# Kernel optimization log

Hardware: AMD Instinct MI355X
Metric: run time of the kernel (lower is better)

## Reference

```python
import jax, jax.numpy as jnp
import numpy as np

B, S, H, F, E, K = 4, 2048, 1024, 2048, 8, 2


def setup_inputs() -> dict:
    key = jax.random.key(0)
    ks = jax.random.split(key, 5)
    scale = 0.02
    return {
        "hidden_states": jax.random.normal(ks[0], (B, S, H), dtype=jnp.float32),
        "gate_w": jax.random.normal(ks[1], (E, H), dtype=jnp.float32) * scale,
        "w1": jax.random.normal(ks[2], (E, F, H), dtype=jnp.float32) * scale,
        "w3": jax.random.normal(ks[3], (E, F, H), dtype=jnp.float32) * scale,
        "w2": jax.random.normal(ks[4], (E, H, F), dtype=jnp.float32) * scale,
    }


def reference(hidden_states, gate_w, w1, w3, w2):
    b, s, h = hidden_states.shape
    x = hidden_states.reshape(-1, h)  # [T, H]
    T = x.shape[0]
    # router
    router_logits = x @ gate_w.T  # [T, E]
    probs = jax.nn.softmax(router_logits.astype(jnp.float32), axis=-1)
    routing_weights, selected = jax.lax.top_k(probs, K)  # [T, K]
    routing_weights = routing_weights / jnp.sum(routing_weights, axis=-1, keepdims=True)
    routing_weights = routing_weights.astype(x.dtype)
    # dense per-token expert weight matrix [T, E] (zero for unselected experts)
    full_w = jnp.zeros((T, gate_w.shape[0]), dtype=x.dtype)
    full_w = full_w.at[jnp.arange(T)[:, None], selected].set(routing_weights)
    out = jnp.zeros_like(x)
    for e in range(gate_w.shape[0]):
        gated = jax.nn.silu(x @ w1[e].T) * (x @ w3[e].T)  # [T, F]
        y = gated @ w2[e].T  # [T, H]
        out = out + full_w[:, e:e + 1] * y
    return out.reshape(b, s, h), router_logits
```

## Files before the change

kernel.cpp:

```cpp
#include <hip/hip_runtime.h>

typedef unsigned short ushort_t;
typedef __attribute__((ext_vector_type(8))) short short8;
typedef __attribute__((ext_vector_type(4))) float floatx4;

#define T_TOK 8192
#define HDIM 1024
#define FDIM 2048
#define NEXP 8
#define TK_SLOTS (T_TOK * 2)
#define SORT_THREADS 1024
#define PER_THREAD (TK_SLOTS / SORT_THREADS)

__device__ __forceinline__ float b2f(unsigned short u) {
    union { unsigned int i; float f; } x; x.i = ((unsigned int)u) << 16; return x.f;
}
__device__ __forceinline__ unsigned short f2b(float f) {
    unsigned int u = __float_as_uint(f);
    u += 0x7FFF + ((u >> 16) & 1);
    return (unsigned short)(u >> 16);
}
__device__ __forceinline__ void gload16(const void* g, void* l) {
    __builtin_amdgcn_global_load_lds((const __attribute__((address_space(1))) void*)g,
                                     (__attribute__((address_space(3))) void*)l,
                                     16, 0, 0);
}

__global__ __launch_bounds__(256) void cvt_kernel(
    const float* __restrict__ src, ushort_t* __restrict__ dst, int n8)
{
    int i = blockIdx.x * 256 + threadIdx.x;
    if (i >= n8) return;
    const float4* s4 = (const float4*)src;
    float4 a = s4[2 * i], b = s4[2 * i + 1];
    short8 o;
    o[0] = (short)f2b(a.x); o[1] = (short)f2b(a.y);
    o[2] = (short)f2b(a.z); o[3] = (short)f2b(a.w);
    o[4] = (short)f2b(b.x); o[5] = (short)f2b(b.y);
    o[6] = (short)f2b(b.z); o[7] = (short)f2b(b.w);
    *(short8*)&dst[(size_t)i * 8] = o;
}

__global__ __launch_bounds__(256) void router_kernel(
    const float* __restrict__ X, const float* __restrict__ GW,
    float* __restrict__ logits_out, int* __restrict__ tk_e,
    float* __restrict__ tk_w)
{
    __shared__ __align__(16) float gw[NEXP * HDIM];
    const int tid = threadIdx.x;
#pragma unroll
    for (int c = 0; c < 8; ++c) {
        int idx = (c * 256 + tid) * 4;
        *(float4*)&gw[idx] = *(const float4*)&GW[idx];
    }
    __syncthreads();
    const int w = tid >> 6, l = tid & 63;
    const int t = blockIdx.x * 4 + w;
    float acc[NEXP];
#pragma unroll
    for (int e = 0; e < NEXP; ++e) acc[e] = 0.f;
#pragma unroll
    for (int it = 0; it < 4; ++it) {
        const int colb = it * 256 + l * 4;
        float4 xv = *(const float4*)&X[(size_t)t * HDIM + colb];
#pragma unroll
        for (int e = 0; e < NEXP; ++e) {
            float4 gv = *(const float4*)&gw[e * HDIM + colb];
            acc[e] += xv.x * gv.x + xv.y * gv.y + xv.z * gv.z + xv.w * gv.w;
        }
    }
#pragma unroll
    for (int off = 32; off >= 1; off >>= 1)
#pragma unroll
        for (int e = 0; e < NEXP; ++e) acc[e] += __shfl_xor(acc[e], off, 64);

    if (l == 0) {
        float mx = acc[0];
#pragma unroll
        for (int e = 1; e < NEXP; ++e) mx = fmaxf(mx, acc[e]);
        float p[NEXP];
#pragma unroll
        for (int e = 0; e < NEXP; ++e) p[e] = __expf(acc[e] - mx);
        int e0 = 0;
#pragma unroll
        for (int e = 1; e < NEXP; ++e) if (p[e] > p[e0]) e0 = e;
        int e1 = (e0 == 0) ? 1 : 0;
#pragma unroll
        for (int e = 0; e < NEXP; ++e) if (e != e0 && p[e] > p[e1]) e1 = e;
        float den = p[e0] + p[e1];
        tk_e[t * 2] = e0; tk_e[t * 2 + 1] = e1;
        tk_w[t * 2] = p[e0] / den; tk_w[t * 2 + 1] = p[e1] / den;
#pragma unroll
        for (int e = 0; e < NEXP; ++e) logits_out[(size_t)t * NEXP + e] = acc[e];
    }
}

__global__ __launch_bounds__(SORT_THREADS) void sort_kernel(
    const int* __restrict__ tk_e, const float* __restrict__ tk_w,
    int* __restrict__ counts, int* __restrict__ offsets,
    int* __restrict__ token_list, float* __restrict__ weight_list,
    int* __restrict__ slot_of)
{
    __shared__ int hist[NEXP][SORT_THREADS];
    __shared__ int offs[NEXP];
    const int thr = threadIdx.x;
    const int base = thr * PER_THREAD;

    int ev[PER_THREAD];
    int cnt[NEXP];
#pragma unroll
    for (int e = 0; e < NEXP; ++e) cnt[e] = 0;
#pragma unroll
    for (int i = 0; i < PER_THREAD; ++i) {
        ev[i] = tk_e[base + i];
#pragma unroll
        for (int e = 0; e < NEXP; ++e) cnt[e] += (ev[i] == e);
    }
#pragma unroll
    for (int e = 0; e < NEXP; ++e) hist[e][thr] = cnt[e];
    __syncthreads();

    for (int off = 1; off < SORT_THREADS; off <<= 1) {
        int v[NEXP];
#pragma unroll
        for (int e = 0; e < NEXP; ++e) v[e] = (thr >= off) ? hist[e][thr - off] : 0;
        __syncthreads();
#pragma unroll
        for (int e = 0; e < NEXP; ++e) hist[e][thr] += v[e];
        __syncthreads();
    }

    if (thr == 0) {
        int s = 0;
#pragma unroll
        for (int e = 0; e < NEXP; ++e) {
            int c = hist[e][SORT_THREADS - 1];
            offs[e] = s; offsets[e] = s; counts[e] = c; s += c;
        }
    }
    __syncthreads();

    int run[NEXP];
#pragma unroll
    for (int e = 0; e < NEXP; ++e) run[e] = offs[e] + hist[e][thr] - cnt[e];

#pragma unroll
    for (int i = 0; i < PER_THREAD; ++i) {
        int e = ev[i];
        int slot = 0;
#pragma unroll
        for (int ee = 0; ee < NEXP; ++ee) if (e == ee) slot = run[ee]++;
        token_list[slot] = (base + i) >> 1;
        weight_list[slot] = tk_w[base + i];
        slot_of[base + i] = slot;
    }
}

template <int MODE, int NDIM, int KDIM, bool GATHER>
__global__ __launch_bounds__(256) void moe_gemm(
    const ushort_t* __restrict__ A, const ushort_t* __restrict__ W,
    const int* __restrict__ counts, const int* __restrict__ offsets,
    const int* __restrict__ token_list, const float* __restrict__ weight_list,
    const ushort_t* C1, ushort_t* Out)
{
    const int e = blockIdx.z;
    const int ne = counts[e];
    const int m0 = blockIdx.y * 128;
    if (m0 >= ne) return;
    const int n0 = blockIdx.x * 128;
    const int aoff = offsets[e];
    const ushort_t* Bw = W + (size_t)e * NDIM * KDIM;

    __shared__ __align__(16) ushort_t As[128 * 32];
    __shared__ __align__(16) ushort_t Bs[128 * 32];

    const int tid = threadIdx.x;
    const int l = tid & 63;
    const int wv = tid >> 6;
    const int wm = wv >> 1, wn = wv & 1;
    const int quad = l >> 4, tl = l & 15;

    floatx4 acc[4][4];
#pragma unroll
    for (int i = 0; i < 4; ++i)
#pragma unroll
        for (int j = 0; j < 4; ++j)
#pragma unroll
            for (int r = 0; r < 4; ++r) acc[i][j][r] = 0.f;

    const ushort_t* agp[2];
    const ushort_t* bgp[2];
    ushort_t* alds[2];
    ushort_t* blds[2];
#pragma unroll
    for (int c = 0; c < 2; ++c) {
        int chunk = c * 256 + tid;
        int row = chunk >> 2, cc = chunk & 3;
        int rowc = m0 + row; if (rowc >= ne) rowc = ne - 1;
        size_t arow = GATHER ? (size_t)token_list[aoff + rowc] : (size_t)(aoff + rowc);
        agp[c] = A + arow * KDIM + cc * 8;
        bgp[c] = Bw + (size_t)(n0 + row) * KDIM + cc * 8;
        int base = (c * 256 + (tid & ~63)) * 8;
        alds[c] = &As[base];
        blds[c] = &Bs[base];
    }

    for (int k0 = 0; k0 < KDIM; k0 += 32) {
        gload16(agp[0] + k0, alds[0]);
        gload16(agp[1] + k0, alds[1]);
        gload16(bgp[0] + k0, blds[0]);
        gload16(bgp[1] + k0, blds[1]);
        __syncthreads();
        short8 a[4], b[4];
#pragma unroll
        for (int i = 0; i < 4; ++i)
            a[i] = *(const short8*)&As[(wm * 64 + i * 16 + tl) * 32 + quad * 8];
#pragma unroll
        for (int j = 0; j < 4; ++j)
            b[j] = *(const short8*)&Bs[(wn * 64 + j * 16 + tl) * 32 + quad * 8];
#pragma unroll
        for (int i = 0; i < 4; ++i)
#pragma unroll
            for (int j = 0; j < 4; ++j)
                acc[i][j] = __builtin_amdgcn_mfma_f32_16x16x32_bf16(a[i], b[j], acc[i][j], 0, 0, 0);
        __syncthreads();
    }

#pragma unroll
    for (int i = 0; i < 4; ++i) {
        int mrow = m0 + wm * 64 + i * 16 + quad * 4;
#pragma unroll
        for (int r = 0; r < 4; ++r) {
            int m = mrow + r;
            if (m < ne) {
                float wgt = 0.f;
                if constexpr (MODE == 2) wgt = weight_list[aoff + m];
#pragma unroll
                for (int j = 0; j < 4; ++j) {
                    int col = n0 + wn * 64 + j * 16 + tl;
                    size_t oidx = (size_t)(aoff + m) * NDIM + col;
                    float v = acc[i][j][r];
                    if constexpr (MODE == 0) {
                        float s = v / (1.f + __expf(-v));
                        Out[oidx] = f2b(s);
                    } else if constexpr (MODE == 1) {
                        float c = b2f(C1[oidx]);
                        Out[oidx] = f2b(v * c);
                    } else {
                        Out[oidx] = f2b(wgt * v);
                    }
                }
            }
        }
    }
}

__global__ __launch_bounds__(256) void combine_kernel(
    const ushort_t* __restrict__ Y, const int* __restrict__ slot_of,
    float* __restrict__ OutF)
{
    int idx = blockIdx.x * 256 + threadIdx.x;
    int t = idx >> 7;
    int h8 = (idx & 127) << 3;
    int s0 = slot_of[t * 2], s1 = slot_of[t * 2 + 1];
    short8 y0 = *(const short8*)&Y[(size_t)s0 * HDIM + h8];
    short8 y1 = *(const short8*)&Y[(size_t)s1 * HDIM + h8];
    float4 o0, o1;
    o0.x = b2f((unsigned short)y0[0]) + b2f((unsigned short)y1[0]);
    o0.y = b2f((unsigned short)y0[1]) + b2f((unsigned short)y1[1]);
    o0.z = b2f((unsigned short)y0[2]) + b2f((unsigned short)y1[2]);
    o0.w = b2f((unsigned short)y0[3]) + b2f((unsigned short)y1[3]);
    o1.x = b2f((unsigned short)y0[4]) + b2f((unsigned short)y1[4]);
    o1.y = b2f((unsigned short)y0[5]) + b2f((unsigned short)y1[5]);
    o1.z = b2f((unsigned short)y0[6]) + b2f((unsigned short)y1[6]);
    o1.w = b2f((unsigned short)y0[7]) + b2f((unsigned short)y1[7]);
    float4* dst = (float4*)&OutF[(size_t)t * HDIM + h8];
    dst[0] = o0; dst[1] = o1;
}

extern "C" void kernel_launch(void* const* d_in, const int* in_sizes, int n_in,
                              void* d_out, int out_size, void* d_ws, size_t ws_size,
                              hipStream_t stream)
{
    const float* X  = (const float*)d_in[0];
    const float* GW = (const float*)d_in[1];
    const float* W1 = (const float*)d_in[2];
    const float* W3 = (const float*)d_in[3];
    const float* W2 = (const float*)d_in[4];
    float* OUT = (float*)d_out;
    float* LOGITS = OUT + (size_t)T_TOK * HDIM;

    char* p = (char*)d_ws;
    auto take = [&](size_t b) { char* q = p; p += (b + 255) & ~(size_t)255; return q; };
    ushort_t* Xb = (ushort_t*)take((size_t)T_TOK * HDIM * 2);
    ushort_t* Wb = (ushort_t*)take((size_t)NEXP * FDIM * HDIM * 2);
    ushort_t* C1 = (ushort_t*)take((size_t)TK_SLOTS * FDIM * 2);
    ushort_t* Yb = (ushort_t*)take((size_t)TK_SLOTS * HDIM * 2);
    int*   counts      = (int*)take(NEXP * 4);
    int*   offsets     = (int*)take(NEXP * 4);
    int*   tk_e        = (int*)take(TK_SLOTS * 4);
    float* tk_w        = (float*)take(TK_SLOTS * 4);
    int*   slot_of     = (int*)take(TK_SLOTS * 4);
    int*   token_list  = (int*)take(TK_SLOTS * 4);
    float* weight_list = (float*)take(TK_SLOTS * 4);

    router_kernel<<<T_TOK / 4, 256, 0, stream>>>(X, GW, LOGITS, tk_e, tk_w);
    sort_kernel<<<1, SORT_THREADS, 0, stream>>>(tk_e, tk_w, counts, offsets,
                                                token_list, weight_list, slot_of);
    cvt_kernel<<<(T_TOK * HDIM / 8) / 256, 256, 0, stream>>>(X, Xb, T_TOK * HDIM / 8);

    cvt_kernel<<<(NEXP * FDIM * HDIM / 8) / 256, 256, 0, stream>>>(W1, Wb, NEXP * FDIM * HDIM / 8);
    moe_gemm<0, FDIM, HDIM, true ><<<dim3(FDIM / 128, T_TOK / 128, NEXP), 256, 0, stream>>>(
        Xb, Wb, counts, offsets, token_list, nullptr, nullptr, C1);

    cvt_kernel<<<(NEXP * FDIM * HDIM / 8) / 256, 256, 0, stream>>>(W3, Wb, NEXP * FDIM * HDIM / 8);
    moe_gemm<1, FDIM, HDIM, true ><<<dim3(FDIM / 128, T_TOK / 128, NEXP), 256, 0, stream>>>(
        Xb, Wb, counts, offsets, token_list, nullptr, C1, C1 );

    cvt_kernel<<<(NEXP * HDIM * FDIM / 8) / 256, 256, 0, stream>>>(W2, Wb, NEXP * HDIM * FDIM / 8);
    moe_gemm<2, HDIM, FDIM, false><<<dim3(HDIM / 128, T_TOK / 128, NEXP), 256, 0, stream>>>(
        C1 , Wb, counts, offsets, token_list, weight_list, nullptr, Yb);

    combine_kernel<<<(T_TOK * HDIM / 8) / 256, 256, 0, stream>>>(Yb, slot_of, OUT);
}
```

Measured before the change: 621.6 us.

## Fuse gate/up GEMMs into one kernel and scatter down-proj via atomics

```diff
diff --git a/kernel.cpp b/kernel.cpp
--- a/kernel.cpp
+++ b/kernel.cpp
@@ -24,6 +24,9 @@
     __builtin_amdgcn_global_load_lds((const __attribute__((address_space(1))) void*)g,
                                      (__attribute__((address_space(3))) void*)l,
                                      16, 0, 0);
+}
+__device__ __forceinline__ void atomAddF(float* p, float v) {
+    __hip_atomic_fetch_add(p, v, __ATOMIC_RELAXED, __HIP_MEMORY_SCOPE_AGENT);
 }
 
 __global__ __launch_bounds__(256) void cvt_kernel(
@@ -98,8 +101,7 @@
 __global__ __launch_bounds__(SORT_THREADS) void sort_kernel(
     const int* __restrict__ tk_e, const float* __restrict__ tk_w,
     int* __restrict__ counts, int* __restrict__ offsets,
-    int* __restrict__ token_list, float* __restrict__ weight_list,
-    int* __restrict__ slot_of)
+    int* __restrict__ token_list, float* __restrict__ weight_list)
 {
     __shared__ int hist[NEXP][SORT_THREADS];
     __shared__ int offs[NEXP];
@@ -152,16 +154,14 @@
         for (int ee = 0; ee < NEXP; ++ee) if (e == ee) slot = run[ee]++;
         token_list[slot] = (base + i) >> 1;
         weight_list[slot] = tk_w[base + i];
-        slot_of[base + i] = slot;
-    }
-}
-
-template <int MODE, int NDIM, int KDIM, bool GATHER>
-__global__ __launch_bounds__(256) void moe_gemm(
-    const ushort_t* __restrict__ A, const ushort_t* __restrict__ W,
+    }
+}
+
+__global__ __launch_bounds__(256) void moe_gemm13(
+    const ushort_t* __restrict__ A, const ushort_t* __restrict__ W1b,
+    const ushort_t* __restrict__ W3b,
     const int* __restrict__ counts, const int* __restrict__ offsets,
-    const int* __restrict__ token_list, const float* __restrict__ weight_list,
-    const ushort_t* C1, ushort_t* Out)
+    const int* __restrict__ token_list, ushort_t* __restrict__ G)
 {
     const int e = blockIdx.z;
     const int ne = counts[e];
@@ -169,10 +169,12 @@
     if (m0 >= ne) return;
     const int n0 = blockIdx.x * 128;
     const int aoff = offsets[e];
-    const ushort_t* Bw = W + (size_t)e * NDIM * KDIM;
+    const ushort_t* B1w = W1b + (size_t)e * FDIM * HDIM;
+    const ushort_t* B3w = W3b + (size_t)e * FDIM * HDIM;
 
     __shared__ __align__(16) ushort_t As[128 * 32];
-    __shared__ __align__(16) ushort_t Bs[128 * 32];
+    __shared__ __align__(16) ushort_t B1s[128 * 32];
+    __shared__ __align__(16) ushort_t B3s[128 * 32];
 
     const int tid = threadIdx.x;
     const int l = tid & 63;
@@ -180,6 +182,106 @@
     const int wm = wv >> 1, wn = wv & 1;
     const int quad = l >> 4, tl = l & 15;
 
+    floatx4 acc1[4][4], acc3[4][4];
+#pragma unroll
+    for (int i = 0; i < 4; ++i)
+#pragma unroll
+        for (int j = 0; j < 4; ++j)
+#pragma unroll
+            for (int r = 0; r < 4; ++r) { acc1[i][j][r] = 0.f; acc3[i][j][r] = 0.f; }
+
+    const ushort_t* agp[2];
+    const ushort_t* b1gp[2];
+    const ushort_t* b3gp[2];
+    ushort_t* alds[2];
+    ushort_t* b1lds[2];
+    ushort_t* b3lds[2];
+#pragma unroll
+    for (int c = 0; c < 2; ++c) {
+        int chunk = c * 256 + tid;
+        int row = chunk >> 2, cc = chunk & 3;
+        int rowc = m0 + row; if (rowc >= ne) rowc = ne - 1;
+        size_t arow = (size_t)token_list[aoff + rowc];
+        agp[c]  = A   + arow * HDIM + cc * 8;
+        b1gp[c] = B1w + (size_t)(n0 + row) * HDIM + cc * 8;
+        b3gp[c] = B3w + (size_t)(n0 + row) * HDIM + cc * 8;
+        int base = (c * 256 + (tid & ~63)) * 8;
+        alds[c]  = &As[base];
+        b1lds[c] = &B1s[base];
+        b3lds[c] = &B3s[base];
+    }
+
+    for (int k0 = 0; k0 < HDIM; k0 += 32) {
+        gload16(agp[0]  + k0, alds[0]);
+        gload16(agp[1]  + k0, alds[1]);
+        gload16(b1gp[0] + k0, b1lds[0]);
+        gload16(b1gp[1] + k0, b1lds[1]);
+        gload16(b3gp[0] + k0, b3lds[0]);
+        gload16(b3gp[1] + k0, b3lds[1]);
+        __syncthreads();
+        short8 a[4], b1[4], b3[4];
+#pragma unroll
+        for (int i = 0; i < 4; ++i)
+            a[i] = *(const short8*)&As[(wm * 64 + i * 16 + tl) * 32 + quad * 8];
+#pragma unroll
+        for (int j = 0; j < 4; ++j) {
+            b1[j] = *(const short8*)&B1s[(wn * 64 + j * 16 + tl) * 32 + quad * 8];
+            b3[j] = *(const short8*)&B3s[(wn * 64 + j * 16 + tl) * 32 + quad * 8];
+        }
+#pragma unroll
+        for (int i = 0; i < 4; ++i)
+#pragma unroll
+            for (int j = 0; j < 4; ++j) {
+                acc1[i][j] = __builtin_amdgcn_mfma_f32_16x16x32_bf16(a[i], b1[j], acc1[i][j], 0, 0, 0);
+                acc3[i][j] = __builtin_amdgcn_mfma_f32_16x16x32_bf16(a[i], b3[j], acc3[i][j], 0, 0, 0);
+            }
+        __syncthreads();
+    }
+
+#pragma unroll
+    for (int i = 0; i < 4; ++i) {
+        int mrow = m0 + wm * 64 + i * 16 + quad * 4;
+#pragma unroll
+        for (int r = 0; r < 4; ++r) {
+            int m = mrow + r;
+            if (m < ne) {
+#pragma unroll
+                for (int j = 0; j < 4; ++j) {
+                    int col = n0 + wn * 64 + j * 16 + tl;
+                    size_t oidx = (size_t)(aoff + m) * FDIM + col;
+                    float v1 = acc1[i][j][r];
+                    float v3 = acc3[i][j][r];
+                    float s = v1 / (1.f + __expf(-v1));
+                    G[oidx] = f2b(s * v3);
+                }
+            }
+        }
+    }
+}
+
+__global__ __launch_bounds__(256) void moe_gemm2(
+    const ushort_t* __restrict__ A , const ushort_t* __restrict__ W2b,
+    const int* __restrict__ counts, const int* __restrict__ offsets,
+    const int* __restrict__ token_list, const float* __restrict__ weight_list,
+    float* __restrict__ OUT)
+{
+    const int e = blockIdx.z;
+    const int ne = counts[e];
+    const int m0 = blockIdx.y * 128;
+    if (m0 >= ne) return;
+    const int n0 = blockIdx.x * 128;
+    const int aoff = offsets[e];
+    const ushort_t* Bw = W2b + (size_t)e * HDIM * FDIM;
+
+    __shared__ __align__(16) ushort_t As[128 * 32];
+    __shared__ __align__(16) ushort_t Bs[128 * 32];
+
+    const int tid = threadIdx.x;
+    const int l = tid & 63;
+    const int wv = tid >> 6;
+    const int wm = wv >> 1, wn = wv & 1;
+    const int quad = l >> 4, tl = l & 15;
+
     floatx4 acc[4][4];
 #pragma unroll
     for (int i = 0; i < 4; ++i)
@@ -197,15 +299,14 @@
         int chunk = c * 256 + tid;
         int row = chunk >> 2, cc = chunk & 3;
         int rowc = m0 + row; if (rowc >= ne) rowc = ne - 1;
-        size_t arow = GATHER ? (size_t)token_list[aoff + rowc] : (size_t)(aoff + rowc);
-        agp[c] = A + arow * KDIM + cc * 8;
-        bgp[c] = Bw + (size_t)(n0 + row) * KDIM + cc * 8;
+        agp[c] = A  + (size_t)(aoff + rowc) * FDIM + cc * 8;
+        bgp[c] = Bw + (size_t)(n0 + row) * FDIM + cc * 8;
         int base = (c * 256 + (tid & ~63)) * 8;
         alds[c] = &As[base];
         blds[c] = &Bs[base];
     }
 
-    for (int k0 = 0; k0 < KDIM; k0 += 32) {
+    for (int k0 = 0; k0 < FDIM; k0 += 32) {
         gload16(agp[0] + k0, alds[0]);
         gload16(agp[1] + k0, alds[1]);
         gload16(bgp[0] + k0, blds[0]);
@@ -233,49 +334,17 @@
         for (int r = 0; r < 4; ++r) {
             int m = mrow + r;
             if (m < ne) {
-                float wgt = 0.f;
-                if constexpr (MODE == 2) wgt = weight_list[aoff + m];
+                float wgt = weight_list[aoff + m];
+                int tok = token_list[aoff + m];
+                float* orow = OUT + (size_t)tok * HDIM;
 #pragma unroll
                 for (int j = 0; j < 4; ++j) {
                     int col = n0 + wn * 64 + j * 16 + tl;
-                    size_t oidx = (size_t)(aoff + m) * NDIM + col;
-                    float v = acc[i][j][r];
-                    if constexpr (MODE == 0) {
-                        float s = v / (1.f + __expf(-v));
-                        Out[oidx] = f2b(s);
-                    } else if constexpr (MODE == 1) {
-                        float c = b2f(C1[oidx]);
-                        Out[oidx] = f2b(v * c);
-                    } else {
-                        Out[oidx] = f2b(wgt * v);
-                    }
+                    atomAddF(&orow[col], wgt * acc[i][j][r]);
                 }
             }
         }
     }
-}
-
-__global__ __launch_bounds__(256) void combine_kernel(
-    const ushort_t* __restrict__ Y, const int* __restrict__ slot_of,
-    float* __restrict__ OutF)
-{
-    int idx = blockIdx.x * 256 + threadIdx.x;
-    int t = idx >> 7;
-    int h8 = (idx & 127) << 3;
-    int s0 = slot_of[t * 2], s1 = slot_of[t * 2 + 1];
-    short8 y0 = *(const short8*)&Y[(size_t)s0 * HDIM + h8];
-    short8 y1 = *(const short8*)&Y[(size_t)s1 * HDIM + h8];
-    float4 o0, o1;
-    o0.x = b2f((unsigned short)y0[0]) + b2f((unsigned short)y1[0]);
-    o0.y = b2f((unsigned short)y0[1]) + b2f((unsigned short)y1[1]);
-    o0.z = b2f((unsigned short)y0[2]) + b2f((unsigned short)y1[2]);
-    o0.w = b2f((unsigned short)y0[3]) + b2f((unsigned short)y1[3]);
-    o1.x = b2f((unsigned short)y0[4]) + b2f((unsigned short)y1[4]);
-    o1.y = b2f((unsigned short)y0[5]) + b2f((unsigned short)y1[5]);
-    o1.z = b2f((unsigned short)y0[6]) + b2f((unsigned short)y1[6]);
-    o1.w = b2f((unsigned short)y0[7]) + b2f((unsigned short)y1[7]);
-    float4* dst = (float4*)&OutF[(size_t)t * HDIM + h8];
-    dst[0] = o0; dst[1] = o1;
 }
 
 extern "C" void kernel_launch(void* const* d_in, const int* in_sizes, int n_in,
@@ -292,34 +361,30 @@
 
     char* p = (char*)d_ws;
     auto take = [&](size_t b) { char* q = p; p += (b + 255) & ~(size_t)255; return q; };
-    ushort_t* Xb = (ushort_t*)take((size_t)T_TOK * HDIM * 2);
-    ushort_t* Wb = (ushort_t*)take((size_t)NEXP * FDIM * HDIM * 2);
-    ushort_t* C1 = (ushort_t*)take((size_t)TK_SLOTS * FDIM * 2);
-    ushort_t* Yb = (ushort_t*)take((size_t)TK_SLOTS * HDIM * 2);
+    ushort_t* Xb  = (ushort_t*)take((size_t)T_TOK * HDIM * 2);
+    ushort_t* W1b = (ushort_t*)take((size_t)NEXP * FDIM * HDIM * 2);
+    ushort_t* W3b = (ushort_t*)take((size_t)NEXP * FDIM * HDIM * 2);
+    ushort_t* C1  = (ushort_t*)take((size_t)TK_SLOTS * FDIM * 2);
     int*   counts      = (int*)take(NEXP * 4);
     int*   offsets     = (int*)take(NEXP * 4);
     int*   tk_e        = (int*)take(TK_SLOTS * 4);
     float* tk_w        = (float*)take(TK_SLOTS * 4);
-    int*   slot_of     = (int*)take(TK_SLOTS * 4);
     int*   token_list  = (int*)take(TK_SLOTS * 4);
     float* weight_list = (float*)take(TK_SLOTS * 4);
 
+    hipMemsetAsync(OUT, 0, (size_t)T_TOK * HDIM * sizeof(float), stream);
+
     router_kernel<<<T_TOK / 4, 256, 0, stream>>>(X, GW, LOGITS, tk_e, tk_w);
     sort_kernel<<<1, SORT_THREADS, 0, stream>>>(tk_e, tk_w, counts, offsets,
-                                                token_list, weight_list, slot_of);
+                                                token_list, weight_list);
     cvt_kernel<<<(T_TOK * HDIM / 8) / 256, 256, 0, stream>>>(X, Xb, T_TOK * HDIM / 8);
-
-    cvt_kernel<<<(NEXP * FDIM * HDIM / 8) / 256, 256, 0, stream>>>(W1, Wb, NEXP * FDIM * HDIM / 8);
-    moe_gemm<0, FDIM, HDIM, true ><<<dim3(FDIM / 128, T_TOK / 128, NEXP), 256, 0, stream>>>(
-        Xb, Wb, counts, offsets, token_list, nullptr, nullptr, C1);
-
-    cvt_kernel<<<(NEXP * FDIM * HDIM / 8) / 256, 256, 0, stream>>>(W3, Wb, NEXP * FDIM * HDIM / 8);
-    moe_gemm<1, FDIM, HDIM, true ><<<dim3(FDIM / 128, T_TOK / 128, NEXP), 256, 0, stream>>>(
-        Xb, Wb, counts, offsets, token_list, nullptr, C1, C1 );
-
-    cvt_kernel<<<(NEXP * HDIM * FDIM / 8) / 256, 256, 0, stream>>>(W2, Wb, NEXP * HDIM * FDIM / 8);
-    moe_gemm<2, HDIM, FDIM, false><<<dim3(HDIM / 128, T_TOK / 128, NEXP), 256, 0, stream>>>(
-        C1 , Wb, counts, offsets, token_list, weight_list, nullptr, Yb);
-
-    combine_kernel<<<(T_TOK * HDIM / 8) / 256, 256, 0, stream>>>(Yb, slot_of, OUT);
-}
+    cvt_kernel<<<(NEXP * FDIM * HDIM / 8) / 256, 256, 0, stream>>>(W1, W1b, NEXP * FDIM * HDIM / 8);
+    cvt_kernel<<<(NEXP * FDIM * HDIM / 8) / 256, 256, 0, stream>>>(W3, W3b, NEXP * FDIM * HDIM / 8);
+
+    moe_gemm13<<<dim3(FDIM / 128, T_TOK / 128, NEXP), 256, 0, stream>>>(
+        Xb, W1b, W3b, counts, offsets, token_list, C1);
+
+    cvt_kernel<<<(NEXP * HDIM * FDIM / 8) / 256, 256, 0, stream>>>(W2, W1b, NEXP * HDIM * FDIM / 8);
+    moe_gemm2<<<dim3(HDIM / 128, T_TOK / 128, NEXP), 256, 0, stream>>>(
+        C1, W1b, counts, offsets, token_list, weight_list, OUT);
+}
```

Result: slower. 743.5 us (+19.6%).
